# Kernel tuning notes

Hardware: AMD Instinct MI355X
Metric: run time of the kernel (lower is better)

The kernel has to match this reference:

```python
import jax, jax.numpy as jnp
import numpy as np

TS = 1.5          # hard-coded sampling period in forward()
W_CENTER = 337.927  # hard-coded center frequency in forward()


def shg_mat(yta):
    """Vectorized createSHGmat: yta is a complex64 vector of length N.
    Row m: Ts * fftshift(fft(fftshift(yta * roll(yta, delay[m]) * shiftFactor))).
    torch.roll(x, s)[j] == x[(j - s) % N], matching the gather below."""
    N = yta.shape[0]
    delays_f = jnp.arange(-(N // 2), N // 2, dtype=jnp.float32)
    delays_i = jnp.arange(-(N // 2), N // 2, dtype=jnp.int32)
    shift_factor = jnp.exp(-1j * 2.0 * W_CENTER * TS * delays_f).astype(jnp.complex64)  # [N]
    idx = (jnp.arange(N, dtype=jnp.int32)[None, :] - delays_i[:, None]) % N  # [N, N]
    y_shift = yta[idx]                                    # [N(delay), N(elem)]
    prod = yta[None, :] * y_shift * shift_factor[None, :]  # elementwise, [N, N]
    prod = jnp.fft.fftshift(prod, axes=-1)
    mat = TS * jnp.fft.fftshift(jnp.fft.fft(prod, axis=-1), axes=-1)
    return mat  # complex64 [N, N]


def frog_error(Tref, Tmeas):
    """calcFrogError: scalar FROG error between reference and measured traces."""
    mu = jnp.sum(Tmeas @ Tref) / jnp.sum(Tref @ Tref)
    r = jnp.sum((Tmeas - mu * Tref) ** 2)
    norm = jnp.float32(Tmeas.size) * jnp.max(Tmeas) ** 2
    return jnp.sqrt(r / norm)


def setup_inputs() -> dict:
    key = jax.random.key(0)
    k1, k2, k3 = jax.random.split(key, 3)
    B, N = 8, 1024
    prediction = jax.random.normal(k1, (B, 2 * N), dtype=jnp.float32)
    label = jax.random.normal(k2, (B, 2 * N), dtype=jnp.float32)
    spectrogram = jax.random.uniform(k3, (N, N), dtype=jnp.float32)
    return {"prediction": prediction, "label": label, "spectrogram": spectrogram}


def reference(prediction, label, spectrogram):
    B, two_n = prediction.shape
    n = two_n // 2
    pred_analytical = (prediction[:, :n] + 1j * prediction[:, n:]).astype(jnp.complex64)  # [B, N]
    mats = jax.vmap(shg_mat)(pred_analytical)          # [B, N, N] complex64
    Tref = jnp.abs(mats)                               # predicted SHG trace magnitude
    errs = jax.vmap(lambda t: frog_error(t, spectrogram))(Tref)  # [B]
    # loss = (sum over batch of frog_error) / batch_size; masked MSE terms in the
    # original are computed but never added to the returned loss, so they are omitted.
    return jnp.mean(errs)
```

## Files before the change

kernel.cpp:

```cpp
#include <hip/hip_runtime.h>
#include <math.h>

#define N 1024
#define B_ 8
#define T_ 256
#define R_ 4
#define NREP 4
#define GX 129

#define OFF_SF      0
#define OFF_TW      2048
#define OFF_ROWSUM  10240
#define ZERO_START  18432
#define OFF_COLSUMM 18432
#define OFF_SUMM2   19456
#define OFF_MAXM    19457
#define OFF_SUMMT   19464
#define OFF_SUMTT   19472
#define OFF_COLT    20480
#define WS_END      (OFF_COLT + B_ * NREP * N)

#define S1(a) ((a) ^ (((a) >> 2) & 0x10))
#define S2(a) ((a) ^ (((a) >> 3) & 0x0C))
#define S3(a) ((a) ^ (((a) >> 5) & 0x07))
#define S4(a) ((a) ^ (((a) >> 5) & 0x07))

__device__ __forceinline__ float wave_sum(float v) {
    #pragma unroll
    for (int o = 32; o > 0; o >>= 1) v += __shfl_down(v, o, 64);
    return v;
}
__device__ __forceinline__ float wave_max(float v) {
    #pragma unroll
    for (int o = 32; o > 0; o >>= 1) v = fmaxf(v, __shfl_down(v, o, 64));
    return v;
}

__device__ __forceinline__ void load_tw(float tw[6], const float* __restrict__ p) {
    float4 v = *(const float4*)p;
    float2 w = *(const float2*)(p + 4);
    tw[0] = v.x; tw[1] = v.y; tw[2] = v.z; tw[3] = v.w; tw[4] = w.x; tw[5] = w.y;
}

__device__ __forceinline__ void bfly4(float xr[4], float xi[4], const float tw[6]) {
    float t0r = xr[0] + xr[2], t0i = xi[0] + xi[2];
    float t1r = xr[0] - xr[2], t1i = xi[0] - xi[2];
    float t2r = xr[1] + xr[3], t2i = xi[1] + xi[3];
    float t3r = xr[1] - xr[3], t3i = xi[1] - xi[3];
    float y1r = t1r + t3i, y1i = t1i - t3r;
    float y2r = t0r - t2r, y2i = t0i - t2i;
    float y3r = t1r - t3i, y3i = t1i + t3r;
    xr[0] = t0r + t2r;            xi[0] = t0i + t2i;
    xr[1] = y1r * tw[0] - y1i * tw[1]; xi[1] = y1r * tw[1] + y1i * tw[0];
    xr[2] = y2r * tw[2] - y2i * tw[3]; xi[2] = y2r * tw[3] + y2i * tw[2];
    xr[3] = y3r * tw[4] - y3i * tw[5]; xi[3] = y3r * tw[5] + y3i * tw[4];
}

__global__ __launch_bounds__(T_) void k_prep(float* ws, float* out) {
    const int e = blockIdx.x * T_ + threadIdx.x;
    {
        double ang = -2.0 * 337.927 * 1.5 * (double)(e - 512);
        double s, c;
        sincos(ang, &s, &c);
        ws[OFF_SF + 2 * e] = (float)c;
        ws[OFF_SF + 2 * e + 1] = (float)s;
    }
    {
        int s = e >> 8, tt = e & 255;
        int h = 256 >> (2 * s);
        int pos = tt & (h - 1);
        int step = 1 << (2 * s);
        double a1 = -2.0 * M_PI * (double)(pos * step) / 1024.0;
        double s1, c1, s2, c2, s3, c3;
        sincos(a1, &s1, &c1);
        sincos(2.0 * a1, &s2, &c2);
        sincos(3.0 * a1, &s3, &c3);
        float* p = ws + OFF_TW + e * 8;
        p[0] = (float)c1; p[1] = (float)s1;
        p[2] = (float)c2; p[3] = (float)s2;
        p[4] = (float)c3; p[5] = (float)s3;
        p[6] = 0.f; p[7] = 0.f;
    }
    for (int j = ZERO_START + e; j < WS_END; j += 4 * T_) ws[j] = 0.f;
    if (e == 0) out[0] = 0.f;
}

__global__ __launch_bounds__(T_, 4) void k_row(const float* __restrict__ pred,
                                               const float* __restrict__ M,
                                               float* __restrict__ ws) {
    __shared__ float Yr[N], Yi[N];
    __shared__ float Ar[N], Ai[N], Br[N], Bi[N];
    __shared__ float colA[N], colM[N];
    __shared__ float red[5][4];
    const int t = threadIdx.x;
    const int blk = blockIdx.x;
    const int b = blockIdx.y;
    const int nr = (blk == GX - 1) ? 1 : R_;
    const int m0 = blk * R_;
    const int wid = t >> 6, lane = t & 63;

    {
        const float* pr = pred + (size_t)b * 2 * N;
        #pragma unroll
        for (int q = 0; q < 4; ++q) {
            int j = t + T_ * q;
            Yr[j] = pr[j];
            Yi[j] = pr[N + j];
            colA[j] = 0.f;
            colM[j] = 0.f;
        }
    }
    __syncthreads();

    float mtacc = 0.f, ttacc = 0.f, sqacc = 0.f, mxacc = 0.f;
    float xr[4], xi[4], tw[6];

    for (int r = 0; r < nr; ++r) {
        const int m = m0 + r;
        const int mm = (N - m) & (N - 1);
        const float w = (mm == m) ? 1.f : 2.f;

        {
            const float2* sf2 = (const float2*)(ws + OFF_SF);
            #pragma unroll
            for (int q = 0; q < 4; ++q) {
                int j = t + T_ * q;
                int s = (j - m + 512) & (N - 1);
                float ar = Yr[j], ai = Yi[j];
                float br = Yr[s], bi = Yi[s];
                float2 sv = sf2[j];
                float p_r = ar * br - ai * bi;
                float p_i = ar * bi + ai * br;
                xr[q] = p_r * sv.x - p_i * sv.y;
                xi[q] = p_r * sv.y + p_i * sv.x;
            }
            load_tw(tw, ws + OFF_TW + (size_t)t * 8);
            bfly4(xr, xi, tw);
            #pragma unroll
            for (int q = 0; q < 4; ++q) { int a = t + 256 * q; Ar[a] = xr[q]; Ai[a] = xi[q]; }
        }
        __syncthreads();

        {
            int base = ((t >> 6) << 8) | (t & 63);
            #pragma unroll
            for (int q = 0; q < 4; ++q) { int a = base + (q << 6); xr[q] = Ar[a]; xi[q] = Ai[a]; }
            load_tw(tw, ws + OFF_TW + (size_t)(256 + t) * 8);
            bfly4(xr, xi, tw);
            #pragma unroll
            for (int q = 0; q < 4; ++q) { int a = S1(base + (q << 6)); Br[a] = xr[q]; Bi[a] = xi[q]; }
        }
        __syncthreads();

        {
            int base = ((t >> 4) << 6) | (t & 15);
            #pragma unroll
            for (int q = 0; q < 4; ++q) { int a = S1(base + (q << 4)); xr[q] = Br[a]; xi[q] = Bi[a]; }
            load_tw(tw, ws + OFF_TW + (size_t)(512 + t) * 8);
            bfly4(xr, xi, tw);
            #pragma unroll
            for (int q = 0; q < 4; ++q) { int a = S2(base + (q << 4)); Ar[a] = xr[q]; Ai[a] = xi[q]; }
        }
        __syncthreads();

        {
            int base = ((t >> 2) << 4) | (t & 3);
            #pragma unroll
            for (int q = 0; q < 4; ++q) { int a = S2(base + (q << 2)); xr[q] = Ar[a]; xi[q] = Ai[a]; }
            load_tw(tw, ws + OFF_TW + (size_t)(768 + t) * 8);
            bfly4(xr, xi, tw);
            #pragma unroll
            for (int q = 0; q < 4; ++q) { int a = S3(base + (q << 2)); Br[a] = xr[q]; Bi[a] = xi[q]; }
        }
        __syncthreads();

        {
            int base = t << 2;
            #pragma unroll
            for (int q = 0; q < 4; ++q) { int a = S3(base + q); xr[q] = Br[a]; xi[q] = Bi[a]; }
            float t0r = xr[0] + xr[2], t0i = xi[0] + xi[2];
            float t1r = xr[0] - xr[2], t1i = xi[0] - xi[2];
            float t2r = xr[1] + xr[3], t2i = xi[1] + xi[3];
            float t3r = xr[1] - xr[3], t3i = xi[1] - xi[3];
            float yr[4], yi[4];
            yr[0] = t0r + t2r; yi[0] = t0i + t2i;
            yr[1] = t1r + t3i; yi[1] = t1i - t3r;
            yr[2] = t0r - t2r; yi[2] = t0i - t2i;
            yr[3] = t1r - t3i; yi[3] = t1i + t3r;
            int r4t = ((t & 3) << 6) | (((t >> 2) & 3) << 4) | (((t >> 4) & 3) << 2) | ((t >> 6) & 3);
            #pragma unroll
            for (int q = 0; q < 4; ++q) {
                int c = ((q << 8) | r4t) ^ 512;
                Ar[S4(c)] = 1.5f * sqrtf(yr[q] * yr[q] + yi[q] * yi[q]);
            }
        }
        __syncthreads();

        {
            const float* Mrow = M + (size_t)m * N;
            const float* Mrow2 = M + (size_t)mm * N;
            float rs = 0.f;
            #pragma unroll
            for (int q = 0; q < 4; ++q) {
                int cc = t + 256 * q;
                float v = Ar[S4(cc)];
                rs += v;
                ttacc += w * v * v;
                float m1 = Mrow[cc];
                float msum = m1;
                if (mm != m) msum += Mrow2[cc];
                mtacc += msum * v;
                colA[cc] += w * v;
                if (b == 0) {
                    colM[cc] += msum;
                    sqacc += m1 * m1;
                    mxacc = fmaxf(mxacc, m1);
                    if (mm != m) {
                        float m2 = msum - m1;
                        sqacc += m2 * m2;
                        mxacc = fmaxf(mxacc, m2);
                    }
                }
            }
            rs = wave_sum(rs);
            if (lane == 0) red[0][wid] = rs;
            __syncthreads();
            if (t == 0) {
                float R = red[0][0] + red[0][1] + red[0][2] + red[0][3];
                ws[OFF_ROWSUM + b * N + m] = R;
                if (mm != m) ws[OFF_ROWSUM + b * N + mm] = R;
            }
        }
    }

    {
        float* colT = ws + OFF_COLT + (size_t)(b * NREP + (blk & (NREP - 1))) * N;
        #pragma unroll
        for (int q = 0; q < 4; ++q) {
            int cc = t + 256 * q;
            atomicAdd(&colT[cc], colA[cc]);
        }
        if (b == 0) {
            #pragma unroll
            for (int q = 0; q < 4; ++q) {
                int cc = t + 256 * q;
                atomicAdd(&ws[OFF_COLSUMM + cc], colM[cc]);
            }
        }
        float mt = wave_sum(mtacc);
        float tt2 = wave_sum(ttacc);
        if (lane == 0) { red[1][wid] = mt; red[2][wid] = tt2; }
        if (b == 0) {
            float sq = wave_sum(sqacc);
            float mx = wave_max(mxacc);
            if (lane == 0) { red[3][wid] = sq; red[4][wid] = mx; }
        }
        __syncthreads();
        if (t == 0) {
            atomicAdd(&ws[OFF_SUMMT + b], red[1][0] + red[1][1] + red[1][2] + red[1][3]);
            atomicAdd(&ws[OFF_SUMTT + b], red[2][0] + red[2][1] + red[2][2] + red[2][3]);
            if (b == 0) {
                atomicAdd(&ws[OFF_SUMM2], red[3][0] + red[3][1] + red[3][2] + red[3][3]);
                float X = fmaxf(fmaxf(red[4][0], red[4][1]), fmaxf(red[4][2], red[4][3]));
                atomicMax((unsigned int*)ws + OFF_MAXM, __float_as_uint(X));
            }
        }
    }
}

__global__ __launch_bounds__(T_) void k_final(float* ws, float* out) {
    __shared__ double redn[4], redd[4];
    const int b = blockIdx.x;
    const int t = threadIdx.x;
    const int wid = t >> 6, lane = t & 63;
    const float* rowsum = ws + OFF_ROWSUM + (size_t)b * N;
    double num = 0.0, den = 0.0;
    #pragma unroll
    for (int q = 0; q < 4; ++q) {
        int j = t + 256 * q;
        double r = (double)rowsum[j];
        float ct = 0.f;
        #pragma unroll
        for (int rep = 0; rep < NREP; ++rep)
            ct += ws[OFF_COLT + (size_t)(b * NREP + rep) * N + j];
        num += (double)ws[OFF_COLSUMM + j] * r;
        den += (double)ct * r;
    }
    #pragma unroll
    for (int o = 32; o > 0; o >>= 1) {
        num += __shfl_down(num, o, 64);
        den += __shfl_down(den, o, 64);
    }
    if (lane == 0) { redn[wid] = num; redd[wid] = den; }
    __syncthreads();
    if (t == 0) {
        double NUM = redn[0] + redn[1] + redn[2] + redn[3];
        double DEN = redd[0] + redd[1] + redd[2] + redd[3];
        double mu = NUM / DEN;
        double r = (double)ws[OFF_SUMM2] - 2.0 * mu * (double)ws[OFF_SUMMT + b]
                 + mu * mu * (double)ws[OFF_SUMTT + b];
        float mx = ws[OFF_MAXM];
        double norm = 1048576.0 * (double)mx * (double)mx;
        atomicAdd(out, (float)(sqrt(r / norm) / 8.0));
    }
}

extern "C" void kernel_launch(void* const* d_in, const int* in_sizes, int n_in,
                              void* d_out, int out_size, void* d_ws, size_t ws_size,
                              hipStream_t stream) {
    const float* pred = (const float*)d_in[0];
    const float* M = (const float*)d_in[2];
    float* ws = (float*)d_ws;
    float* out = (float*)d_out;

    k_prep<<<4, T_, 0, stream>>>(ws, out);
    dim3 grid(GX, B_);
    k_row<<<grid, T_, 0, stream>>>(pred, M, ws);
    k_final<<<B_, T_, 0, stream>>>(ws, out);
}
```

Measured before the change: 105.3 us.

## Offload spectrogram statistics to extra blocks and hoist twiddle loads

Moves the spectrogram column sum, sum of squares and max out of the batch-0 FFT blocks into a separate extra grid row of 64 blocks, so the batch-0 blocks no longer carry extra divergent work. It also hoists the four twiddle loads out of the row loop into registers, defers per-row sum writes to the end of the block to remove a barrier, and raises the launch-bounds occupancy hint from 4 to 6. This trades extra register pressure and added launched blocks (most of which exit immediately) for a more even load.

```diff
diff --git a/kernel.cpp b/kernel.cpp
--- a/kernel.cpp
+++ b/kernel.cpp
@@ -85,19 +85,49 @@
     if (e == 0) out[0] = 0.f;
 }
 
-__global__ __launch_bounds__(T_, 4) void k_row(const float* __restrict__ pred,
+__global__ __launch_bounds__(T_, 6) void k_row(const float* __restrict__ pred,
                                                const float* __restrict__ M,
                                                float* __restrict__ ws) {
     __shared__ float Yr[N], Yi[N];
     __shared__ float Ar[N], Ai[N], Br[N], Bi[N];
-    __shared__ float colA[N], colM[N];
-    __shared__ float red[5][4];
+    __shared__ float colA[N];
+    __shared__ float red[R_ + 2][4];
     const int t = threadIdx.x;
     const int blk = blockIdx.x;
     const int b = blockIdx.y;
+    const int wid = t >> 6, lane = t & 63;
+
+    if (b == B_) {
+        if (blk >= 64) return;
+        const int r0 = blk * 16;
+        float cs[4] = {0.f, 0.f, 0.f, 0.f};
+        float sq = 0.f, mx = 0.f;
+        for (int r = 0; r < 16; ++r) {
+            const float* row = M + (size_t)(r0 + r) * N;
+            #pragma unroll
+            for (int q = 0; q < 4; ++q) {
+                float v = row[t + T_ * q];
+                cs[q] += v;
+                sq += v * v;
+                mx = fmaxf(mx, v);
+            }
+        }
+        #pragma unroll
+        for (int q = 0; q < 4; ++q) atomicAdd(&ws[OFF_COLSUMM + t + T_ * q], cs[q]);
+        sq = wave_sum(sq);
+        mx = wave_max(mx);
+        if (lane == 0) { red[0][wid] = sq; red[1][wid] = mx; }
+        __syncthreads();
+        if (t == 0) {
+            atomicAdd(&ws[OFF_SUMM2], red[0][0] + red[0][1] + red[0][2] + red[0][3]);
+            float X = fmaxf(fmaxf(red[1][0], red[1][1]), fmaxf(red[1][2], red[1][3]));
+            atomicMax((unsigned int*)ws + OFF_MAXM, __float_as_uint(X));
+        }
+        return;
+    }
+
     const int nr = (blk == GX - 1) ? 1 : R_;
     const int m0 = blk * R_;
-    const int wid = t >> 6, lane = t & 63;
 
     {
         const float* pr = pred + (size_t)b * 2 * N;
@@ -107,13 +137,18 @@
             Yr[j] = pr[j];
             Yi[j] = pr[N + j];
             colA[j] = 0.f;
-            colM[j] = 0.f;
-        }
-    }
+        }
+    }
+
+    float tw0[6], tw1[6], tw2[6], tw3[6];
+    load_tw(tw0, ws + OFF_TW + (size_t)t * 8);
+    load_tw(tw1, ws + OFF_TW + (size_t)(256 + t) * 8);
+    load_tw(tw2, ws + OFF_TW + (size_t)(512 + t) * 8);
+    load_tw(tw3, ws + OFF_TW + (size_t)(768 + t) * 8);
     __syncthreads();
 
-    float mtacc = 0.f, ttacc = 0.f, sqacc = 0.f, mxacc = 0.f;
-    float xr[4], xi[4], tw[6];
+    float mtacc = 0.f, ttacc = 0.f;
+    float xr[4], xi[4];
 
     for (int r = 0; r < nr; ++r) {
         const int m = m0 + r;
@@ -134,8 +169,7 @@
                 xr[q] = p_r * sv.x - p_i * sv.y;
                 xi[q] = p_r * sv.y + p_i * sv.x;
             }
-            load_tw(tw, ws + OFF_TW + (size_t)t * 8);
-            bfly4(xr, xi, tw);
+            bfly4(xr, xi, tw0);
             #pragma unroll
             for (int q = 0; q < 4; ++q) { int a = t + 256 * q; Ar[a] = xr[q]; Ai[a] = xi[q]; }
         }
@@ -145,8 +179,7 @@
             int base = ((t >> 6) << 8) | (t & 63);
             #pragma unroll
             for (int q = 0; q < 4; ++q) { int a = base + (q << 6); xr[q] = Ar[a]; xi[q] = Ai[a]; }
-            load_tw(tw, ws + OFF_TW + (size_t)(256 + t) * 8);
-            bfly4(xr, xi, tw);
+            bfly4(xr, xi, tw1);
             #pragma unroll
             for (int q = 0; q < 4; ++q) { int a = S1(base + (q << 6)); Br[a] = xr[q]; Bi[a] = xi[q]; }
         }
@@ -156,8 +189,7 @@
             int base = ((t >> 4) << 6) | (t & 15);
             #pragma unroll
             for (int q = 0; q < 4; ++q) { int a = S1(base + (q << 4)); xr[q] = Br[a]; xi[q] = Bi[a]; }
-            load_tw(tw, ws + OFF_TW + (size_t)(512 + t) * 8);
-            bfly4(xr, xi, tw);
+            bfly4(xr, xi, tw2);
             #pragma unroll
             for (int q = 0; q < 4; ++q) { int a = S2(base + (q << 4)); Ar[a] = xr[q]; Ai[a] = xi[q]; }
         }
@@ -167,8 +199,7 @@
             int base = ((t >> 2) << 4) | (t & 3);
             #pragma unroll
             for (int q = 0; q < 4; ++q) { int a = S2(base + (q << 2)); xr[q] = Ar[a]; xi[q] = Ai[a]; }
-            load_tw(tw, ws + OFF_TW + (size_t)(768 + t) * 8);
-            bfly4(xr, xi, tw);
+            bfly4(xr, xi, tw3);
             #pragma unroll
             for (int q = 0; q < 4; ++q) { int a = S3(base + (q << 2)); Br[a] = xr[q]; Bi[a] = xi[q]; }
         }
@@ -206,31 +237,15 @@
                 float v = Ar[S4(cc)];
                 rs += v;
                 ttacc += w * v * v;
-                float m1 = Mrow[cc];
-                float msum = m1;
+                float msum = Mrow[cc];
                 if (mm != m) msum += Mrow2[cc];
                 mtacc += msum * v;
                 colA[cc] += w * v;
-                if (b == 0) {
-                    colM[cc] += msum;
-                    sqacc += m1 * m1;
-                    mxacc = fmaxf(mxacc, m1);
-                    if (mm != m) {
-                        float m2 = msum - m1;
-                        sqacc += m2 * m2;
-                        mxacc = fmaxf(mxacc, m2);
-                    }
-                }
             }
             rs = wave_sum(rs);
-            if (lane == 0) red[0][wid] = rs;
-            __syncthreads();
-            if (t == 0) {
-                float R = red[0][0] + red[0][1] + red[0][2] + red[0][3];
-                ws[OFF_ROWSUM + b * N + m] = R;
-                if (mm != m) ws[OFF_ROWSUM + b * N + mm] = R;
-            }
-        }
+            if (lane == 0) red[r][wid] = rs;
+        }
+        __syncthreads();
     }
 
     {
@@ -240,30 +255,19 @@
             int cc = t + 256 * q;
             atomicAdd(&colT[cc], colA[cc]);
         }
-        if (b == 0) {
-            #pragma unroll
-            for (int q = 0; q < 4; ++q) {
-                int cc = t + 256 * q;
-                atomicAdd(&ws[OFF_COLSUMM + cc], colM[cc]);
-            }
-        }
         float mt = wave_sum(mtacc);
         float tt2 = wave_sum(ttacc);
-        if (lane == 0) { red[1][wid] = mt; red[2][wid] = tt2; }
-        if (b == 0) {
-            float sq = wave_sum(sqacc);
-            float mx = wave_max(mxacc);
-            if (lane == 0) { red[3][wid] = sq; red[4][wid] = mx; }
-        }
+        if (lane == 0) { red[R_][wid] = mt; red[R_ + 1][wid] = tt2; }
         __syncthreads();
         if (t == 0) {
-            atomicAdd(&ws[OFF_SUMMT + b], red[1][0] + red[1][1] + red[1][2] + red[1][3]);
-            atomicAdd(&ws[OFF_SUMTT + b], red[2][0] + red[2][1] + red[2][2] + red[2][3]);
-            if (b == 0) {
-                atomicAdd(&ws[OFF_SUMM2], red[3][0] + red[3][1] + red[3][2] + red[3][3]);
-                float X = fmaxf(fmaxf(red[4][0], red[4][1]), fmaxf(red[4][2], red[4][3]));
-                atomicMax((unsigned int*)ws + OFF_MAXM, __float_as_uint(X));
-            }
+            for (int r = 0; r < nr; ++r) {
+                int m = m0 + r, mm = (N - m) & (N - 1);
+                float R = red[r][0] + red[r][1] + red[r][2] + red[r][3];
+                ws[OFF_ROWSUM + b * N + m] = R;
+                if (mm != m) ws[OFF_ROWSUM + b * N + mm] = R;
+            }
+            atomicAdd(&ws[OFF_SUMMT + b], red[R_][0] + red[R_][1] + red[R_][2] + red[R_][3]);
+            atomicAdd(&ws[OFF_SUMTT + b], red[R_ + 1][0] + red[R_ + 1][1] + red[R_ + 1][2] + red[R_ + 1][3]);
         }
     }
 }
@@ -314,7 +318,7 @@
     float* out = (float*)d_out;
 
     k_prep<<<4, T_, 0, stream>>>(ws, out);
-    dim3 grid(GX, B_);
+    dim3 grid(GX, B_ + 1);
     k_row<<<grid, T_, 0, stream>>>(pred, M, ws);
     k_final<<<B_, T_, 0, stream>>>(ws, out);
 }
```

After: 100.9 us. 4.2% less time.
